# Kernel tuning notes

Measured on AMD Instinct MI355X. Metric: run time of the kernel, lower is better.

## Reference

```python
import jax, jax.numpy as jnp
from jax import lax
import numpy as np

NB_CODE = 16384
DIM = 128
SCALES = [(1, 1), (2, 2), (4, 4), (8, 8), (16, 16)]
PHI_IDX = [0, 1, 1, 2, 3]  # PhiPartiallyShared: argmin(|ticks - si/(SN-1)|), K=4, SN=5
RESI = 0.5  # abs(quant_resi)
BETA = 0.25


def _cubic(x, a=-0.75):
    # PyTorch bicubic kernel (cubic convolution, a=-0.75)
    ax = np.abs(x)
    return np.where(ax <= 1.0, (a + 2.0) * ax ** 3 - (a + 3.0) * ax ** 2 + 1.0,
                    np.where(ax < 2.0, a * ax ** 3 - 5.0 * a * ax ** 2 + 8.0 * a * ax - 4.0 * a, 0.0))


def bicubic_mat(n_in, n_out):
    # 1D interpolation matrix matching torch F.interpolate(mode='bicubic', align_corners=False)
    W = np.zeros((n_out, n_in), dtype=np.float32)
    scale = n_in / n_out
    for i in range(n_out):
        x = (i + 0.5) * scale - 0.5
        x0 = int(np.floor(x))
        t = x - x0
        for k in range(4):
            idx = min(max(x0 - 1 + k, 0), n_in - 1)  # border clamp
            W[i, idx] += _cubic(t + 1.0 - k)
    return jnp.asarray(W)


def phi_apply(h, w, b):
    y = lax.conv_general_dilated(h, w, (1, 1), 'SAME',
                                 dimension_numbers=('NCHW', 'OIHW', 'NCHW'))
    y = y + b[None, :, None, None]
    return h * (1.0 - RESI) + y * RESI


def setup_inputs() -> dict:
    key = jax.random.key(0)
    k1, k2, k3, k4 = jax.random.split(key, 4)
    B, C, J, L = 16, DIM, 16, 16
    f_bcjl = jax.random.normal(k1, (B, C, J, L), dtype=jnp.float32)
    emb = jax.random.normal(k2, (NB_CODE, C), dtype=jnp.float32) * 0.02
    # 4 partially-shared Phi convs (3x3, C->C)
    phi_w = jax.random.normal(k3, (4, C, C, 3, 3), dtype=jnp.float32) * (1.0 / np.sqrt(C * 9))
    phi_b = jax.random.normal(k4, (4, C), dtype=jnp.float32) * 0.01
    return {'f_bcjl': f_bcjl, 'emb': emb, 'phi_w': phi_w, 'phi_b': phi_b}


def reference(f_bcjl, emb, phi_w, phi_b):
    B, C, J, L = f_bcjl.shape
    SN = len(SCALES)
    f_ng = lax.stop_gradient(f_bcjl)
    f_rest = f_ng
    f_hat = jnp.zeros_like(f_ng)
    loss = jnp.float32(0.0)
    e_sq = jnp.sum(emb * emb, axis=1)  # [K]
    idx_all = []
    for si, (sn, tn) in enumerate(SCALES):
        if si != SN - 1:
            # 'area' downsample == integer-factor average pooling here
            r = f_rest.reshape(B, C, sn, J // sn, tn, L // tn).mean(axis=(3, 5))
        else:
            r = f_rest
        rNC = r.transpose(0, 2, 3, 1).reshape(-1, C)  # [N, C]
        d = jnp.sum(rNC * rNC, axis=1, keepdims=True) + e_sq - 2.0 * (rNC @ emb.T)
        idx = jnp.argmin(d, axis=1)  # [N]
        idx_all.append(idx)
        h = emb[idx].reshape(B, sn, tn, C).transpose(0, 3, 1, 2)  # [B,C,sn,tn]
        if si != SN - 1:
            Wj = bicubic_mat(sn, J)
            Wl = bicubic_mat(tn, L)
            h = jnp.einsum('js,bcst,lt->bcjl', Wj, h, Wl)
        k = PHI_IDX[si]
        h = phi_apply(h, phi_w[k], phi_b[k])
        f_hat = f_hat + h
        f_rest = f_rest - h
        loss = loss + BETA * jnp.mean((lax.stop_gradient(f_hat) - f_bcjl) ** 2) \
                    + jnp.mean((f_hat - f_ng) ** 2)
    loss = loss / SN
    idx_cat = jnp.concatenate(idx_all)
    counts = jnp.zeros((NB_CODE,), jnp.float32).at[idx_cat].add(1.0)
    p = counts / idx_cat.shape[0]
    perplexity = jnp.exp(-jnp.sum(p * jnp.log(p + 1e-10)))
    # straight-through estimator
    f_hat_out = lax.stop_gradient(f_hat) - f_ng + f_bcjl
    return (f_hat_out, loss, perplexity)
```

## Files before the change

### kernel.cpp

```cpp
#include <hip/hip_runtime.h>
#include <hip/hip_bf16.h>
#include <math.h>

#define BATCH 16
#define CDIM  128
#define NCODE 16384
#define ELEMS 524288
#define NTOT  5456
#define WEXT_TOT 589824
#define LOSS_COEF 4.76837158203125e-7f

typedef __attribute__((ext_vector_type(8))) short short8;
typedef __attribute__((ext_vector_type(4))) float float4v;
typedef unsigned short ushortT;
typedef unsigned long long u64;
typedef unsigned int u32;

__device__ __forceinline__ ushortT f2bf(float x) {
    __hip_bfloat16 h = __float2bfloat16(x);
    return *reinterpret_cast<ushortT*>(&h);
}
__device__ __forceinline__ float bf2f(ushortT b) {
    __hip_bfloat16 h = *reinterpret_cast<__hip_bfloat16*>(&b);
    return __bfloat162float(h);
}
__device__ __forceinline__ u32 ford(float v) {
    u32 b = __float_as_uint(v);
    return b ^ ((u32)((int)b >> 31) | 0x80000000u);
}

__device__ double cubic_d(double x) {
    const double a = -0.75;
    double ax = fabs(x);
    if (ax <= 1.0) return (a + 2.0) * ax * ax * ax - (a + 3.0) * ax * ax + 1.0;
    if (ax < 2.0)  return a * ax * ax * ax - 5.0 * a * ax * ax + 8.0 * a * ax - 4.0 * a;
    return 0.0;
}

__global__ __launch_bounds__(256)
void k_prologue(const float* __restrict__ f, const float* __restrict__ emb,
                const float* __restrict__ phi_w,
                float* __restrict__ f_rest, float* __restrict__ f_hat,
                float* __restrict__ esq, ushortT* __restrict__ embext,
                ushortT* __restrict__ wext, float* __restrict__ wmat,
                float* __restrict__ lossA) {
    const int t = threadIdx.x;
    const int id = blockIdx.x * 256 + t;

    if (id < ELEMS) {
        f_rest[id] = f[id];
        f_hat[id] = 0.f;
        int row = id >> 5, c4 = id & 31;
        float4 v = reinterpret_cast<const float4*>(emb + (size_t)row * CDIM)[c4];
        float xs[4] = {v.x, v.y, v.z, v.w};
        ushortT hi[4], lo[4];
        float ss = 0.f;
        #pragma unroll
        for (int i = 0; i < 4; ++i) {
            hi[i] = f2bf(xs[i]);
            lo[i] = f2bf(xs[i] - bf2f(hi[i]));
            ss += xs[i] * xs[i];
        }
        ushortT* base = embext + (size_t)row * 256;
        *reinterpret_cast<ushort4*>(base + c4 * 4)       = make_ushort4(hi[0], hi[1], hi[2], hi[3]);
        *reinterpret_cast<ushort4*>(base + 128 + c4 * 4) = make_ushort4(lo[0], lo[1], lo[2], lo[3]);
        #pragma unroll
        for (int off = 16; off; off >>= 1) ss += __shfl_down(ss, off);
        if ((t & 31) == 0) esq[row] = ss;
    }
    if (id < WEXT_TOT) {
        int k4 = id / 147456, rem = id % 147456;
        int co = rem / 1152, kk = rem % 1152;
        int off = kk >> 7, ci = kk & 127;
        float v = 0.5f * phi_w[(((size_t)(k4 * 128 + co)) * 128 + ci) * 9 + off];
        if (ci == co && off == 4) v += 0.5f;
        wext[id] = f2bf(v);
    }
    if (blockIdx.x == 0 && t < 64) {
        int sIdx = t >> 4;
        int S = 1 << sIdx;
        int j = t & 15;
        const int offs[4] = {0, 16, 48, 112};
        double row[8];
        for (int s = 0; s < 8; ++s) row[s] = 0.0;
        double scale = (double)S / 16.0;
        double x = (j + 0.5) * scale - 0.5;
        double x0 = floor(x);
        double tt = x - x0;
        for (int k = 0; k < 4; ++k) {
            int idx = (int)x0 - 1 + k;
            idx = idx < 0 ? 0 : (idx > S - 1 ? S - 1 : idx);
            row[idx] += cubic_d(tt + 1.0 - k);
        }
        for (int s = 0; s < S; ++s) wmat[offs[sIdx] + j * S + s] = (float)row[s];
    }
    if (id == 0) lossA[0] = 0.f;
}

__global__ __launch_bounds__(256)
void k_packext(const float* __restrict__ fr, ushortT* __restrict__ re,
               u64* __restrict__ packed, int N, int padN, int S, int lgS) {
    int id = blockIdx.x * 256 + threadIdx.x;
    if (id < N) packed[id] = ~0ull;
    if (id >= padN * 32) return;
    int row = id >> 5, c4 = id & 31;
    ushortT hi[4], lo[4];
    if (row < N) {
        int mask = S - 1;
        int tt = row & mask, ssi = (row >> lgS) & mask, b = row >> (2 * lgS);
        int bs = 16 >> lgS;
        float inv = 1.f / (float)(bs * bs);
        #pragma unroll
        for (int u = 0; u < 4; ++u) {
            int c = c4 * 4 + u;
            const float* base = fr + (size_t)(b * 128 + c) * 256 + (ssi * bs) * 16 + tt * bs;
            float acc = 0.f;
            for (int jj = 0; jj < bs; ++jj)
                for (int ll = 0; ll < bs; ++ll)
                    acc += base[jj * 16 + ll];
            float x = acc * inv;
            hi[u] = f2bf(x);
            lo[u] = f2bf(x - bf2f(hi[u]));
        }
    } else {
        #pragma unroll
        for (int u = 0; u < 4; ++u) { hi[u] = 0; lo[u] = 0; }
    }
    ushortT* base = re + (size_t)row * 256;
    *reinterpret_cast<ushort4*>(base + c4 * 4)       = make_ushort4(hi[0], hi[1], hi[2], hi[3]);
    *reinterpret_cast<ushort4*>(base + 128 + c4 * 4) = make_ushort4(lo[0], lo[1], lo[2], lo[3]);
}

__global__ __launch_bounds__(256)
void k_packext_wave(const float* __restrict__ fr, ushortT* __restrict__ re,
                    u64* __restrict__ packed, int N, int padN, int S, int lgS) {
    int gid = blockIdx.x * 256 + threadIdx.x;
    int wid = gid >> 6, lane = threadIdx.x & 63;
    if (wid >= padN * 128) return;
    int row = wid >> 7, c = wid & 127;
    float x = 0.f;
    if (row < N) {
        int mask = S - 1;
        int tt = row & mask, ssi = (row >> lgS) & mask, b = row >> (2 * lgS);
        int lgbs = 4 - lgS, bs = 1 << lgbs, cnt = bs * bs;
        const float* base = fr + (size_t)(b * 128 + c) * 256 + (ssi * bs) * 16 + tt * bs;
        float acc = 0.f;
        for (int e = lane; e < cnt; e += 64)
            acc += base[(e >> lgbs) * 16 + (e & (bs - 1))];
        #pragma unroll
        for (int off = 32; off; off >>= 1) acc += __shfl_down(acc, off);
        x = acc / (float)cnt;
    }
    if (lane == 0) {
        ushortT h = f2bf(x);
        re[(size_t)row * 256 + c] = h;
        re[(size_t)row * 256 + 128 + c] = f2bf(x - bf2f(h));
        if (c == 0 && row < N) packed[row] = ~0ull;
    }
}

__global__ __launch_bounds__(256)
void k_argmin_mfma(const ushortT* __restrict__ rext, const ushortT* __restrict__ embext,
                   const float* __restrict__ esq, int N, int kPerSplit,
                   u64* __restrict__ packed) {
    __shared__ ushortT Btile[64 * 32 * 8];
    const int t = threadIdx.x;
    const int w = t >> 6;
    const int lane = t & 63;
    const int ln = lane & 15;
    const int q  = lane >> 4;
    const int k0beg = blockIdx.y * kPerSplit;
    const int rowW = blockIdx.x * 128 + w * 32;

    short8 a[2][8];
    {
        const ushortT* r0 = rext + (size_t)(rowW + ln) * 256 + q * 8;
        const ushortT* r1 = rext + (size_t)(rowW + 16 + ln) * 256 + q * 8;
        #pragma unroll
        for (int sb = 0; sb < 8; ++sb) {
            a[0][sb] = *reinterpret_cast<const short8*>(r0 + sb * 32);
            a[1][sb] = *reinterpret_cast<const short8*>(r1 + sb * 32);
        }
    }

    float minv[2][4];
    int   mini[2][4];
    #pragma unroll
    for (int tt = 0; tt < 2; ++tt)
        #pragma unroll
        for (int rg = 0; rg < 4; ++rg) { minv[tt][rg] = 3.4e38f; mini[tt][rg] = 0; }

    for (int k0 = k0beg; k0 < k0beg + kPerSplit; k0 += 64) {
        __syncthreads();
        #pragma unroll
        for (int i = 0; i < 8; ++i) {
            int F = (i * 4 + w) * 64 + lane;
            int n = F >> 5, cs = F & 31;
            int cp = (cs & ~7) | ((cs & 7) ^ (n & 7));
            const ushortT* src = embext + (size_t)(k0 + n) * 256 + cp * 8;
            __builtin_amdgcn_global_load_lds(
                (const __attribute__((address_space(1))) unsigned int*)src,
                (__attribute__((address_space(3))) unsigned int*)&Btile[(size_t)((i * 4 + w) * 64) * 8],
                16, 0, 0);
        }
        __syncthreads();

        #pragma unroll
        for (int sub = 0; sub < 4; ++sub) {
            int n = sub * 16 + ln;
            short8 bfr[8];
            #pragma unroll
            for (int sb = 0; sb < 8; ++sb) {
                int cp = q + 4 * sb;
                int cs = (cp & ~7) | ((cp & 7) ^ (n & 7));
                bfr[sb] = *reinterpret_cast<const short8*>(&Btile[(size_t)(n * 32 + cs) * 8]);
            }
            float4v acc0 = {0.f, 0.f, 0.f, 0.f};
            float4v acc1 = {0.f, 0.f, 0.f, 0.f};
            #pragma unroll
            for (int s = 0; s < 12; ++s) {
                int as = s < 8 ? s : s - 8;
                int bs = s < 4 ? s : s - 4;
                acc0 = __builtin_amdgcn_mfma_f32_16x16x32_bf16(a[0][as], bfr[bs], acc0, 0, 0, 0);
                acc1 = __builtin_amdgcn_mfma_f32_16x16x32_bf16(a[1][as], bfr[bs], acc1, 0, 0, 0);
            }
            int kc = k0 + sub * 16 + ln;
            float es = esq[kc];
            #pragma unroll
            for (int rg = 0; rg < 4; ++rg) {
                float sc0 = fmaf(-2.f, acc0[rg], es);
                if (sc0 < minv[0][rg]) { minv[0][rg] = sc0; mini[0][rg] = kc; }
                float sc1 = fmaf(-2.f, acc1[rg], es);
                if (sc1 < minv[1][rg]) { minv[1][rg] = sc1; mini[1][rg] = kc; }
            }
        }
    }

    #pragma unroll
    for (int tt = 0; tt < 2; ++tt)
        #pragma unroll
        for (int rg = 0; rg < 4; ++rg) {
            float v = minv[tt][rg]; int ix = mini[tt][rg];
            #pragma unroll
            for (int off = 1; off < 16; off <<= 1) {
                float ov = __shfl_xor(v, off);
                int   oi = __shfl_xor(ix, off);
                if (ov < v || (ov == v && oi < ix)) { v = ov; ix = oi; }
            }
            if (ln == 0) {
                int row = rowW + tt * 16 + q * 4 + rg;
                if (row < N) {
                    u64 p = ((u64)ford(v) << 32) | (u32)ix;
                    atomicMin(&packed[row], p);
                }
            }
        }
}

__global__ __launch_bounds__(256)
void k_upsample(const float* __restrict__ emb, const u64* __restrict__ packed,
                const float* __restrict__ wm, int S, ushortT* __restrict__ h_bf) {
    const int bj = blockIdx.x;
    const int b = bj >> 4, j = bj & 15;
    const int t = threadIdx.x;
    const int l = t >> 4, cs = t & 15;
    float acc[8];
    #pragma unroll
    for (int i = 0; i < 8; ++i) acc[i] = 0.f;
    for (int s = 0; s < S; ++s) {
        float wjv = wm[j * S + s];
        for (int tt = 0; tt < S; ++tt) {
            float wv = wjv * wm[l * S + tt];
            int n = (b * S + s) * S + tt;
            int idx = (int)(u32)(packed[n] & 0xFFFFFFFFull);
            const float* er = emb + (size_t)idx * CDIM + cs * 8;
            float4 e0 = *reinterpret_cast<const float4*>(er);
            float4 e1 = *reinterpret_cast<const float4*>(er + 4);
            acc[0] += wv * e0.x; acc[1] += wv * e0.y;
            acc[2] += wv * e0.z; acc[3] += wv * e0.w;
            acc[4] += wv * e1.x; acc[5] += wv * e1.y;
            acc[6] += wv * e1.z; acc[7] += wv * e1.w;
        }
    }
    int phys = (cs & 8) | ((cs & 7) ^ (l & 7));
    short8 o;
    #pragma unroll
    for (int i = 0; i < 8; ++i) o[i] = (short)f2bf(acc[i]);
    *reinterpret_cast<short8*>(&h_bf[((size_t)(b * 256 + j * 16 + l) * 16 + phys) * 8]) = o;
}

__global__ __launch_bounds__(256)
void k_gather16(const float* __restrict__ emb, const u64* __restrict__ packed,
                ushortT* __restrict__ h_bf) {
    int id = blockIdx.x * 256 + threadIdx.x;
    int cs = id & 15, l = (id >> 4) & 15, j = (id >> 8) & 15, b = id >> 12;
    int n = (b * 16 + j) * 16 + l;
    int idx = (int)(u32)(packed[n] & 0xFFFFFFFFull);
    const float* er = emb + (size_t)idx * CDIM + cs * 8;
    float4 e0 = *reinterpret_cast<const float4*>(er);
    float4 e1 = *reinterpret_cast<const float4*>(er + 4);
    float v[8] = {e0.x, e0.y, e0.z, e0.w, e1.x, e1.y, e1.z, e1.w};
    int phys = (cs & 8) | ((cs & 7) ^ (l & 7));
    short8 o;
    #pragma unroll
    for (int i = 0; i < 8; ++i) o[i] = (short)f2bf(v[i]);
    *reinterpret_cast<short8*>(&h_bf[((size_t)(b * 256 + j * 16 + l) * 16 + phys) * 8]) = o;
}

__global__ __launch_bounds__(128)
void k_convmm(const ushortT* __restrict__ h_bf, const ushortT* __restrict__ wext,
              const float* __restrict__ bias, const float* __restrict__ f_in,
              float* __restrict__ f_hat, float* __restrict__ f_rest,
              float* __restrict__ loss_acc) {
    __shared__ __align__(16) ushortT Htile[3 * 16 * 128];
    __shared__ float wsum[2];
    const int t = threadIdx.x;
    const int w = t >> 6, lane = t & 63;
    const int ln = lane & 15, q = lane >> 4;
    const int ch = blockIdx.x & 1;
    const int j  = (blockIdx.x >> 1) & 15;
    const int b  = blockIdx.x >> 5;

    #pragma unroll
    for (int i = 0; i < 6; ++i) {
        int Fb = i * 128 + w * 64;
        int sr = Fb >> 8;
        int jin = j - 1 + sr;
        if (jin >= 0 && jin < 16) {
            int rc = (Fb & 255) + lane;
            const ushortT* src = h_bf + ((size_t)(b * 256 + jin * 16) * 16) * 8 + (size_t)rc * 8;
            __builtin_amdgcn_global_load_lds(
                (const __attribute__((address_space(1))) unsigned int*)src,
                (__attribute__((address_space(3))) unsigned int*)&Htile[(size_t)Fb * 8],
                16, 0, 0);
        } else {
            *reinterpret_cast<float4*>(&Htile[(size_t)(Fb + lane) * 8]) =
                make_float4(0.f, 0.f, 0.f, 0.f);
        }
    }
    __syncthreads();

    const int co0 = ch * 64 + w * 32;
    const ushortT* wA = wext + (size_t)(co0 + ln) * 1152;
    float4v acc[2] = {{0.f, 0.f, 0.f, 0.f}, {0.f, 0.f, 0.f, 0.f}};
    const short8 zz = {0, 0, 0, 0, 0, 0, 0, 0};

    #pragma unroll 3
    for (int off = 0; off < 9; ++off) {
        const int dj = off / 3, dl = off % 3;
        int cIn = ln + dl - 1;
        int cCl = cIn < 0 ? 0 : (cIn > 15 ? 15 : cIn);
        bool oob = (cIn != cCl);
        int rb = (dj * 16 + cCl) * 128;
        #pragma unroll
        for (int g = 0; g < 4; ++g) {
            int csl = g * 4 + q;
            int phys = (csl & 8) | ((csl & 7) ^ (cCl & 7));
            short8 av = *reinterpret_cast<const short8*>(&Htile[rb + phys * 8]);
            if (oob) av = zz;
            const ushortT* wr = wA + (off * 4 + g) * 32 + q * 8;
            short8 b0 = *reinterpret_cast<const short8*>(wr);
            short8 b1 = *reinterpret_cast<const short8*>(wr + 16 * 1152);
            acc[0] = __builtin_amdgcn_mfma_f32_16x16x32_bf16(av, b0, acc[0], 0, 0, 0);
            acc[1] = __builtin_amdgcn_mfma_f32_16x16x32_bf16(av, b1, acc[1], 0, 0, 0);
        }
    }

    float s = 0.f;
    #pragma unroll
    for (int sn = 0; sn < 2; ++sn) {
        int co = co0 + sn * 16 + ln;
        float bsv = 0.5f * bias[co];
        size_t gi = ((size_t)(b * 128 + co) * 16 + j) * 16 + q * 4;
        float4 fh = *reinterpret_cast<const float4*>(&f_hat[gi]);
        float4 fr = *reinterpret_cast<const float4*>(&f_rest[gi]);
        float4 fv = *reinterpret_cast<const float4*>(&f_in[gi]);
        float o0 = acc[sn][0] + bsv, o1 = acc[sn][1] + bsv;
        float o2 = acc[sn][2] + bsv, o3 = acc[sn][3] + bsv;
        fh.x += o0; fh.y += o1; fh.z += o2; fh.w += o3;
        fr.x -= o0; fr.y -= o1; fr.z -= o2; fr.w -= o3;
        *reinterpret_cast<float4*>(&f_hat[gi]) = fh;
        *reinterpret_cast<float4*>(&f_rest[gi]) = fr;
        float d0 = fh.x - fv.x, d1 = fh.y - fv.y;
        float d2 = fh.z - fv.z, d3 = fh.w - fv.w;
        s += d0 * d0 + d1 * d1 + d2 * d2 + d3 * d3;
    }
    #pragma unroll
    for (int off = 32; off; off >>= 1) s += __shfl_down(s, off);
    if (lane == 0) wsum[w] = s;
    __syncthreads();
    if (t == 0) atomicAdd(loss_acc, (wsum[0] + wsum[1]) * LOSS_COEF);
}

__global__ __launch_bounds__(256)
void k_final(const u64* __restrict__ packed, const float* __restrict__ loss_acc,
             float* __restrict__ out) {
    __shared__ u32 cnt2[NCODE / 2];
    __shared__ float ws4[4];
    int t = threadIdx.x;
    for (int i = t; i < NCODE / 2; i += 256) cnt2[i] = 0;
    __syncthreads();
    for (int i = t; i < NTOT; i += 256) {
        int idx = (int)(u32)(packed[i] & 0xFFFFFFFFull);
        atomicAdd(&cnt2[idx >> 1], (idx & 1) ? 65536u : 1u);
    }
    __syncthreads();
    float s = 0.f;
    for (int k = t; k < NCODE; k += 256) {
        u32 c = cnt2[k >> 1];
        c = (k & 1) ? (c >> 16) : (c & 0xFFFFu);
        float p = (float)c * (1.0f / (float)NTOT);
        s += p * logf(p + 1e-10f);
    }
    #pragma unroll
    for (int off = 32; off; off >>= 1) s += __shfl_down(s, off);
    if ((t & 63) == 0) ws4[t >> 6] = s;
    __syncthreads();
    if (t == 0) {
        out[ELEMS]     = loss_acc[0];
        out[ELEMS + 1] = expf(-(ws4[0] + ws4[1] + ws4[2] + ws4[3]));
    }
}

extern "C" void kernel_launch(void* const* d_in, const int* in_sizes, int n_in,
                              void* d_out, int out_size, void* d_ws, size_t ws_size,
                              hipStream_t stream) {
    const float* f     = (const float*)d_in[0];
    const float* emb   = (const float*)d_in[1];
    const float* phi_w = (const float*)d_in[2];
    const float* phi_b = (const float*)d_in[3];
    float* out = (float*)d_out;

    float* wsf = (float*)d_ws;
    float*   f_rest = wsf;
    ushortT* h_bf   = (ushortT*)(wsf + 524288);
    float*   esq    = wsf + 786432;
    float*   wmat   = wsf + 802816;
    float*   lossA  = wsf + 803072;
    u64*     packed = (u64*)(wsf + 803136);
    ushortT* embext = (ushortT*)(wsf + 819520);
    ushortT* rext   = (ushortT*)(wsf + 2916672);
    ushortT* wext   = (ushortT*)(wsf + 3440960);

    k_prologue<<<2304, 256, 0, stream>>>(f, emb, phi_w, f_rest, out, esq,
                                         embext, wext, wmat, lossA);

    const int Ss[5]     = {1, 2, 4, 8, 16};
    const int lgSs[5]   = {0, 1, 2, 3, 4};
    const int phiIdx[5] = {0, 1, 1, 2, 3};
    const int ksplit[5] = {256, 256, 256, 128, 32};
    const int wmOff[5]  = {0, 16, 48, 112, 0};
    const int pOff[5]   = {0, 16, 80, 336, 1360};

    for (int si = 0; si < 5; ++si) {
        int S = Ss[si], lgS = lgSs[si];
        int N = 16 * S * S;
        int padN = (N + 127) & ~127;
        u64* pk = packed + pOff[si];

        if (S <= 2)
            k_packext_wave<<<padN * 128 / 4, 256, 0, stream>>>(f_rest, rext, pk, N, padN, S, lgS);
        else
            k_packext<<<padN * 32 / 256, 256, 0, stream>>>(f_rest, rext, pk, N, padN, S, lgS);

        int KS = ksplit[si];
        k_argmin_mfma<<<dim3(padN / 128, KS), 256, 0, stream>>>(rext, embext, esq,
                                                                N, NCODE / KS, pk);

        if (si < 4)
            k_upsample<<<256, 256, 0, stream>>>(emb, pk, wmat + wmOff[si], S, h_bf);
        else
            k_gather16<<<256, 256, 0, stream>>>(emb, pk, h_bf);

        int k = phiIdx[si];
        k_convmm<<<512, 128, 0, stream>>>(h_bf, wext + (size_t)k * 147456,
                                          phi_b + (size_t)k * 128, f, out, f_rest, lossA);
    }

    k_final<<<1, 256, 0, stream>>>(packed, lossA, out);
}
```

Before: 392.2 us.

## Fuse upsample/gather into conv kernel and double-buffer argmin codebook tiles

Merges the bicubic upsample or gather step into the conv kernel. Each block now builds its three needed input rows in shared memory directly, which removes the h_bf round trip through global memory and one launch per scale. The argmin kernel double-buffers its codebook tiles so the next tile's global-to-LDS load overlaps the current tile's MFMA work. The K-split counts are halved for the later scales, which gives fewer blocks and longer loops. In exchange, the conv blocks now redo the upsample for neighbouring rows (three times the upsample work), and the grid is 256 blocks of 256 threads instead of 512 of 128.

```diff
diff --git a/kernel.cpp b/kernel.cpp
--- a/kernel.cpp
+++ b/kernel.cpp
@@ -163,7 +163,7 @@
 void k_argmin_mfma(const ushortT* __restrict__ rext, const ushortT* __restrict__ embext,
                    const float* __restrict__ esq, int N, int kPerSplit,
                    u64* __restrict__ packed) {
-    __shared__ ushortT Btile[64 * 32 * 8];
+    __shared__ ushortT Btile[2][64 * 32 * 8];
     const int t = threadIdx.x;
     const int w = t >> 6;
     const int lane = t & 63;
@@ -190,20 +190,39 @@
         #pragma unroll
         for (int rg = 0; rg < 4; ++rg) { minv[tt][rg] = 3.4e38f; mini[tt][rg] = 0; }
 
-    for (int k0 = k0beg; k0 < k0beg + kPerSplit; k0 += 64) {
+    const int tiles = kPerSplit >> 6;
+
+    #pragma unroll
+    for (int i = 0; i < 8; ++i) {
+        int F = (i * 4 + w) * 64 + lane;
+        int n = F >> 5, cs = F & 31;
+        int cp = (cs & ~7) | ((cs & 7) ^ (n & 7));
+        const ushortT* src = embext + (size_t)(k0beg + n) * 256 + cp * 8;
+        __builtin_amdgcn_global_load_lds(
+            (const __attribute__((address_space(1))) unsigned int*)src,
+            (__attribute__((address_space(3))) unsigned int*)&Btile[0][(size_t)((i * 4 + w) * 64) * 8],
+            16, 0, 0);
+    }
+
+    for (int it = 0; it < tiles; ++it) {
         __syncthreads();
-        #pragma unroll
-        for (int i = 0; i < 8; ++i) {
-            int F = (i * 4 + w) * 64 + lane;
-            int n = F >> 5, cs = F & 31;
-            int cp = (cs & ~7) | ((cs & 7) ^ (n & 7));
-            const ushortT* src = embext + (size_t)(k0 + n) * 256 + cp * 8;
-            __builtin_amdgcn_global_load_lds(
-                (const __attribute__((address_space(1))) unsigned int*)src,
-                (__attribute__((address_space(3))) unsigned int*)&Btile[(size_t)((i * 4 + w) * 64) * 8],
-                16, 0, 0);
-        }
-        __syncthreads();
+        if (it + 1 < tiles) {
+            int k1 = k0beg + (it + 1) * 64;
+            int bu = (it + 1) & 1;
+            #pragma unroll
+            for (int i = 0; i < 8; ++i) {
+                int F = (i * 4 + w) * 64 + lane;
+                int n = F >> 5, cs = F & 31;
+                int cp = (cs & ~7) | ((cs & 7) ^ (n & 7));
+                const ushortT* src = embext + (size_t)(k1 + n) * 256 + cp * 8;
+                __builtin_amdgcn_global_load_lds(
+                    (const __attribute__((address_space(1))) unsigned int*)src,
+                    (__attribute__((address_space(3))) unsigned int*)&Btile[bu][(size_t)((i * 4 + w) * 64) * 8],
+                    16, 0, 0);
+            }
+        }
+        const ushortT* Bt = Btile[it & 1];
+        const int k0 = k0beg + it * 64;
 
         #pragma unroll
         for (int sub = 0; sub < 4; ++sub) {
@@ -213,7 +232,7 @@
             for (int sb = 0; sb < 8; ++sb) {
                 int cp = q + 4 * sb;
                 int cs = (cp & ~7) | ((cp & 7) ^ (n & 7));
-                bfr[sb] = *reinterpret_cast<const short8*>(&Btile[(size_t)(n * 32 + cs) * 8]);
+                bfr[sb] = *reinterpret_cast<const short8*>(&Bt[(size_t)(n * 32 + cs) * 8]);
             }
             float4v acc0 = {0.f, 0.f, 0.f, 0.f};
             float4v acc1 = {0.f, 0.f, 0.f, 0.f};
@@ -258,91 +277,62 @@
 }
 
 __global__ __launch_bounds__(256)
-void k_upsample(const float* __restrict__ emb, const u64* __restrict__ packed,
-                const float* __restrict__ wm, int S, ushortT* __restrict__ h_bf) {
-    const int bj = blockIdx.x;
-    const int b = bj >> 4, j = bj & 15;
+void k_upconv(const float* __restrict__ emb, const u64* __restrict__ packed,
+              const float* __restrict__ wm, int S, int lastScale,
+              const ushortT* __restrict__ wext, const float* __restrict__ bias,
+              const float* __restrict__ f_in, float* __restrict__ f_hat,
+              float* __restrict__ f_rest, float* __restrict__ loss_acc) {
+    __shared__ __align__(16) ushortT Htile[3 * 16 * 128];
+    __shared__ float wsum[4];
     const int t = threadIdx.x;
-    const int l = t >> 4, cs = t & 15;
-    float acc[8];
-    #pragma unroll
-    for (int i = 0; i < 8; ++i) acc[i] = 0.f;
-    for (int s = 0; s < S; ++s) {
-        float wjv = wm[j * S + s];
-        for (int tt = 0; tt < S; ++tt) {
-            float wv = wjv * wm[l * S + tt];
-            int n = (b * S + s) * S + tt;
-            int idx = (int)(u32)(packed[n] & 0xFFFFFFFFull);
-            const float* er = emb + (size_t)idx * CDIM + cs * 8;
-            float4 e0 = *reinterpret_cast<const float4*>(er);
-            float4 e1 = *reinterpret_cast<const float4*>(er + 4);
-            acc[0] += wv * e0.x; acc[1] += wv * e0.y;
-            acc[2] += wv * e0.z; acc[3] += wv * e0.w;
-            acc[4] += wv * e1.x; acc[5] += wv * e1.y;
-            acc[6] += wv * e1.z; acc[7] += wv * e1.w;
-        }
-    }
-    int phys = (cs & 8) | ((cs & 7) ^ (l & 7));
-    short8 o;
-    #pragma unroll
-    for (int i = 0; i < 8; ++i) o[i] = (short)f2bf(acc[i]);
-    *reinterpret_cast<short8*>(&h_bf[((size_t)(b * 256 + j * 16 + l) * 16 + phys) * 8]) = o;
-}
-
-__global__ __launch_bounds__(256)
-void k_gather16(const float* __restrict__ emb, const u64* __restrict__ packed,
-                ushortT* __restrict__ h_bf) {
-    int id = blockIdx.x * 256 + threadIdx.x;
-    int cs = id & 15, l = (id >> 4) & 15, j = (id >> 8) & 15, b = id >> 12;
-    int n = (b * 16 + j) * 16 + l;
-    int idx = (int)(u32)(packed[n] & 0xFFFFFFFFull);
-    const float* er = emb + (size_t)idx * CDIM + cs * 8;
-    float4 e0 = *reinterpret_cast<const float4*>(er);
-    float4 e1 = *reinterpret_cast<const float4*>(er + 4);
-    float v[8] = {e0.x, e0.y, e0.z, e0.w, e1.x, e1.y, e1.z, e1.w};
-    int phys = (cs & 8) | ((cs & 7) ^ (l & 7));
-    short8 o;
-    #pragma unroll
-    for (int i = 0; i < 8; ++i) o[i] = (short)f2bf(v[i]);
-    *reinterpret_cast<short8*>(&h_bf[((size_t)(b * 256 + j * 16 + l) * 16 + phys) * 8]) = o;
-}
-
-__global__ __launch_bounds__(128)
-void k_convmm(const ushortT* __restrict__ h_bf, const ushortT* __restrict__ wext,
-              const float* __restrict__ bias, const float* __restrict__ f_in,
-              float* __restrict__ f_hat, float* __restrict__ f_rest,
-              float* __restrict__ loss_acc) {
-    __shared__ __align__(16) ushortT Htile[3 * 16 * 128];
-    __shared__ float wsum[2];
-    const int t = threadIdx.x;
+    const int b = blockIdx.x >> 4;
+    const int j = blockIdx.x & 15;
+
+    {
+        const int l = t >> 4, c8 = t & 15;
+        const int phys = (c8 & 8) | ((c8 & 7) ^ (l & 7));
+        #pragma unroll
+        for (int r = 0; r < 3; ++r) {
+            int jin = j - 1 + r;
+            float acc[8] = {0.f, 0.f, 0.f, 0.f, 0.f, 0.f, 0.f, 0.f};
+            if (jin >= 0 && jin < 16) {
+                if (lastScale) {
+                    int idx = (int)(u32)(packed[(b * 16 + jin) * 16 + l] & 0xFFFFFFFFull);
+                    const float* er = emb + (size_t)idx * CDIM + c8 * 8;
+                    float4 e0 = *reinterpret_cast<const float4*>(er);
+                    float4 e1 = *reinterpret_cast<const float4*>(er + 4);
+                    acc[0] = e0.x; acc[1] = e0.y; acc[2] = e0.z; acc[3] = e0.w;
+                    acc[4] = e1.x; acc[5] = e1.y; acc[6] = e1.z; acc[7] = e1.w;
+                } else {
+                    for (int s = 0; s < S; ++s) {
+                        float wjv = wm[jin * S + s];
+                        for (int tt2 = 0; tt2 < S; ++tt2) {
+                            float wv = wjv * wm[l * S + tt2];
+                            int idx = (int)(u32)(packed[(b * S + s) * S + tt2] & 0xFFFFFFFFull);
+                            const float* er = emb + (size_t)idx * CDIM + c8 * 8;
+                            float4 e0 = *reinterpret_cast<const float4*>(er);
+                            float4 e1 = *reinterpret_cast<const float4*>(er + 4);
+                            acc[0] += wv * e0.x; acc[1] += wv * e0.y;
+                            acc[2] += wv * e0.z; acc[3] += wv * e0.w;
+                            acc[4] += wv * e1.x; acc[5] += wv * e1.y;
+                            acc[6] += wv * e1.z; acc[7] += wv * e1.w;
+                        }
+                    }
+                }
+            }
+            short8 o;
+            #pragma unroll
+            for (int i = 0; i < 8; ++i) o[i] = (short)f2bf(acc[i]);
+            *reinterpret_cast<short8*>(&Htile[((size_t)(r * 16 + l) * 16 + phys) * 8]) = o;
+        }
+    }
+    __syncthreads();
+
     const int w = t >> 6, lane = t & 63;
     const int ln = lane & 15, q = lane >> 4;
-    const int ch = blockIdx.x & 1;
-    const int j  = (blockIdx.x >> 1) & 15;
-    const int b  = blockIdx.x >> 5;
-
-    #pragma unroll
-    for (int i = 0; i < 6; ++i) {
-        int Fb = i * 128 + w * 64;
-        int sr = Fb >> 8;
-        int jin = j - 1 + sr;
-        if (jin >= 0 && jin < 16) {
-            int rc = (Fb & 255) + lane;
-            const ushortT* src = h_bf + ((size_t)(b * 256 + jin * 16) * 16) * 8 + (size_t)rc * 8;
-            __builtin_amdgcn_global_load_lds(
-                (const __attribute__((address_space(1))) unsigned int*)src,
-                (__attribute__((address_space(3))) unsigned int*)&Htile[(size_t)Fb * 8],
-                16, 0, 0);
-        } else {
-            *reinterpret_cast<float4*>(&Htile[(size_t)(Fb + lane) * 8]) =
-                make_float4(0.f, 0.f, 0.f, 0.f);
-        }
-    }
-    __syncthreads();
-
-    const int co0 = ch * 64 + w * 32;
+    const int co0 = w * 32;
     const ushortT* wA = wext + (size_t)(co0 + ln) * 1152;
-    float4v acc[2] = {{0.f, 0.f, 0.f, 0.f}, {0.f, 0.f, 0.f, 0.f}};
+    float4v acc2[2] = {{0.f, 0.f, 0.f, 0.f}, {0.f, 0.f, 0.f, 0.f}};
     const short8 zz = {0, 0, 0, 0, 0, 0, 0, 0};
 
     #pragma unroll 3
@@ -361,8 +351,8 @@
             const ushortT* wr = wA + (off * 4 + g) * 32 + q * 8;
             short8 b0 = *reinterpret_cast<const short8*>(wr);
             short8 b1 = *reinterpret_cast<const short8*>(wr + 16 * 1152);
-            acc[0] = __builtin_amdgcn_mfma_f32_16x16x32_bf16(av, b0, acc[0], 0, 0, 0);
-            acc[1] = __builtin_amdgcn_mfma_f32_16x16x32_bf16(av, b1, acc[1], 0, 0, 0);
+            acc2[0] = __builtin_amdgcn_mfma_f32_16x16x32_bf16(av, b0, acc2[0], 0, 0, 0);
+            acc2[1] = __builtin_amdgcn_mfma_f32_16x16x32_bf16(av, b1, acc2[1], 0, 0, 0);
         }
     }
 
@@ -375,8 +365,8 @@
         float4 fh = *reinterpret_cast<const float4*>(&f_hat[gi]);
         float4 fr = *reinterpret_cast<const float4*>(&f_rest[gi]);
         float4 fv = *reinterpret_cast<const float4*>(&f_in[gi]);
-        float o0 = acc[sn][0] + bsv, o1 = acc[sn][1] + bsv;
-        float o2 = acc[sn][2] + bsv, o3 = acc[sn][3] + bsv;
+        float o0 = acc2[sn][0] + bsv, o1 = acc2[sn][1] + bsv;
+        float o2 = acc2[sn][2] + bsv, o3 = acc2[sn][3] + bsv;
         fh.x += o0; fh.y += o1; fh.z += o2; fh.w += o3;
         fr.x -= o0; fr.y -= o1; fr.z -= o2; fr.w -= o3;
         *reinterpret_cast<float4*>(&f_hat[gi]) = fh;
@@ -389,7 +379,8 @@
     for (int off = 32; off; off >>= 1) s += __shfl_down(s, off);
     if (lane == 0) wsum[w] = s;
     __syncthreads();
-    if (t == 0) atomicAdd(loss_acc, (wsum[0] + wsum[1]) * LOSS_COEF);
+    if (t == 0)
+        atomicAdd(loss_acc, (wsum[0] + wsum[1] + wsum[2] + wsum[3]) * LOSS_COEF);
 }
 
 __global__ __launch_bounds__(256)
@@ -433,14 +424,13 @@
 
     float* wsf = (float*)d_ws;
     float*   f_rest = wsf;
-    ushortT* h_bf   = (ushortT*)(wsf + 524288);
-    float*   esq    = wsf + 786432;
-    float*   wmat   = wsf + 802816;
-    float*   lossA  = wsf + 803072;
-    u64*     packed = (u64*)(wsf + 803136);
-    ushortT* embext = (ushortT*)(wsf + 819520);
-    ushortT* rext   = (ushortT*)(wsf + 2916672);
-    ushortT* wext   = (ushortT*)(wsf + 3440960);
+    float*   esq    = wsf + 524288;
+    float*   wmat   = wsf + 540672;
+    float*   lossA  = wsf + 540928;
+    u64*     packed = (u64*)(wsf + 540992);
+    ushortT* embext = (ushortT*)(wsf + 557376);
+    ushortT* rext   = (ushortT*)(wsf + 2654528);
+    ushortT* wext   = (ushortT*)(wsf + 3178816);
 
     k_prologue<<<2304, 256, 0, stream>>>(f, emb, phi_w, f_rest, out, esq,
                                          embext, wext, wmat, lossA);
@@ -448,7 +438,7 @@
     const int Ss[5]     = {1, 2, 4, 8, 16};
     const int lgSs[5]   = {0, 1, 2, 3, 4};
     const int phiIdx[5] = {0, 1, 1, 2, 3};
-    const int ksplit[5] = {256, 256, 256, 128, 32};
+    const int ksplit[5] = {256, 256, 128, 64, 16};
     const int wmOff[5]  = {0, 16, 48, 112, 0};
     const int pOff[5]   = {0, 16, 80, 336, 1360};
 
@@ -467,13 +457,9 @@
         k_argmin_mfma<<<dim3(padN / 128, KS), 256, 0, stream>>>(rext, embext, esq,
                                                                 N, NCODE / KS, pk);
 
-        if (si < 4)
-            k_upsample<<<256, 256, 0, stream>>>(emb, pk, wmat + wmOff[si], S, h_bf);
-        else
-            k_gather16<<<256, 256, 0, stream>>>(emb, pk, h_bf);
-
         int k = phiIdx[si];
-        k_convmm<<<512, 128, 0, stream>>>(h_bf, wext + (size_t)k * 147456,
+        k_upconv<<<256, 256, 0, stream>>>(emb, pk, wmat + wmOff[si], S, si == 4 ? 1 : 0,
+                                          wext + (size_t)k * 147456,
                                           phi_b + (size_t)k * 128, f, out, f_rest, lossA);
     }
 
```

New measurement: 358.4 us. 8.6% less time.
